# Kernel tuning notes

Hardware: AMD Instinct MI355X
Metric: run time of the kernel (lower is better)

The kernel has to match this reference:

```python
import jax, jax.numpy as jnp
import numpy as np

MAX_SEQ_LEN = 1024
EMBED_DIM = 64


def setup_inputs() -> dict:
    key = jax.random.key(0)
    k1, k2, k3 = jax.random.split(key, 3)
    B, H, L, D = 2, 16, 1024, EMBED_DIM
    q = jax.random.normal(k1, (B, H, L, D), dtype=jnp.float32)
    k = jax.random.normal(k2, (B, H, L, D), dtype=jnp.float32)
    pos_emb = jax.random.normal(k3, (2 * MAX_SEQ_LEN - 1, D), dtype=jnp.float32)
    return {"q": q, "k": k, "pos_emb": pos_emb}


def reference(q, k, pos_emb):
    q_len = q.shape[2]
    k_len = k.shape[2]
    # relative distance index matrix, shifted and clamped into table range
    idx = jnp.arange(q_len)[:, None] - jnp.arange(k_len)[None, :] + (MAX_SEQ_LEN - 1)
    idx = jnp.clip(idx, 0, 2 * MAX_SEQ_LEN - 2)
    rel_emb = pos_emb[idx]  # [q_len, k_len, D]  (the O(Q*K*D) gather)
    # per-query batched contraction over head dim D
    bias = jnp.einsum('bhqd,qkd->bhqk', q, rel_emb)
    return bias / jnp.sqrt(jnp.asarray(EMBED_DIM, dtype=q.dtype))
```

## Files before the change

### kernel.cpp

```cpp
#include <hip/hip_runtime.h>
#include <hip/hip_bf16.h>
#include <stdint.h>


#define LSEQ 1024
#define DDIM 64

typedef __attribute__((ext_vector_type(8))) short bf16x8;
typedef __attribute__((ext_vector_type(16))) float f32x16;

__device__ __forceinline__ unsigned short f2b(float f) {
  union { float f; unsigned u; } c; c.f = f;
  unsigned u = c.u;
  u += 0x7fffu + ((u >> 16) & 1u);
  return (unsigned short)(u >> 16);
}

__global__ __launch_bounds__(256) void cvt_p_kernel(
    const float4* __restrict__ p4, ushort4* __restrict__ pb) {
  int j = blockIdx.x * 256 + threadIdx.x;
  if (j < 32752) {
    float4 v = p4[j];
    ushort4 o;
    o.x = f2b(v.x); o.y = f2b(v.y); o.z = f2b(v.z); o.w = f2b(v.w);
    pb[j] = o;
  }
}

__global__ __launch_bounds__(256) void rpe_kernel(
    const float* __restrict__ Qf, const short* __restrict__ Pb,
    float* __restrict__ out) {
  __shared__ short lds[4][2][2048];
  const int bid  = (int)blockIdx.x;
  const int q    = ((bid & 7) << 7) + (bid >> 3);
  const int tid  = (int)threadIdx.x;
  const int lane = tid & 63;
  const int wave = tid >> 6;
  const int l31  = lane & 31;
  const int hi   = lane >> 5;
  const int nbase = wave << 8;

  const int lane_off = ((lane >> 3) << 7) + ((((lane & 7) ^ (lane >> 3))) << 4);
  const char* Pc = (const char*)Pb;

  auto STAGE = [&](int tt, int buf) {
    const int lo = q + 992 - nbase - (tt << 5);
    const char* src = Pc + ((size_t)lo << 7) + lane_off;
#pragma unroll
    for (int j = 0; j < 4; ++j)
      __builtin_amdgcn_global_load_lds(
          (const __attribute__((address_space(1))) void*)(src + (j << 10)),
          (__attribute__((address_space(3))) void*)&lds[wave][buf][j << 9],
          16, 0, 0);
  };

  STAGE(0, 0);

  bf16x8 a[4];
  {
    const float* qp = Qf + ((size_t)((l31 << 10) + q)) * DDIM + (hi << 3);
#pragma unroll
    for (int s = 0; s < 4; ++s) {
      float4 u = *(const float4*)(qp + 16 * s);
      float4 v = *(const float4*)(qp + 16 * s + 4);
      bf16x8 t;
      t[0] = (short)f2b(u.x * 0.125f); t[1] = (short)f2b(u.y * 0.125f);
      t[2] = (short)f2b(u.z * 0.125f); t[3] = (short)f2b(u.w * 0.125f);
      t[4] = (short)f2b(v.x * 0.125f); t[5] = (short)f2b(v.y * 0.125f);
      t[6] = (short)f2b(v.z * 0.125f); t[7] = (short)f2b(v.w * 0.125f);
      a[s] = t;
    }
  }

  STAGE(1, 1);

  const int rr = 31 - l31;
  const int rx = rr & 7;

  f32x16 accA, accB;
#pragma unroll
  for (int t = 0; t < 8; ++t) {
    if (t == 0 || t == 1)
      asm volatile("s_waitcnt vmcnt(4)" ::: "memory");
    else if (t == 7)
      asm volatile("s_waitcnt vmcnt(32)" ::: "memory");
    else
      asm volatile("s_waitcnt vmcnt(36)" ::: "memory");

    f32x16& acc = (t & 1) ? accB : accA;
#pragma unroll
    for (int r = 0; r < 16; ++r) acc[r] = 0.0f;

    const short* base = &lds[wave][t & 1][rr << 6];
#pragma unroll
    for (int s = 0; s < 4; ++s) {
      bf16x8 bfr = *(const bf16x8*)(base + (((hi + 2 * s) ^ rx) << 3));
      acc = __builtin_amdgcn_mfma_f32_32x32x16_bf16(a[s], bfr, acc, 0, 0, 0);
    }

    if (t < 6) STAGE(t + 2, t & 1);

    if (t & 1) {
      float* ob = out + ((size_t)hi << 22) + (q << 10) + nbase + ((t - 1) << 5) + l31;
#pragma unroll
      for (int r = 0; r < 16; ++r) {
        const int m = (r & 3) + 8 * (r >> 2);
        ob[(size_t)m << 20]        = accA[r];
        ob[((size_t)m << 20) + 32] = accB[r];
      }
    }
  }
}

extern "C" void kernel_launch(void* const* d_in, const int* in_sizes, int n_in,
                              void* d_out, int out_size, void* d_ws, size_t ws_size,
                              hipStream_t stream) {
  const float* qin = (const float*)d_in[0];
  const float* pin = (const float*)d_in[2];

  short* pb = (short*)d_ws;

  cvt_p_kernel<<<128, 256, 0, stream>>>((const float4*)pin, (ushort4*)pb);
  rpe_kernel<<<1024, 256, 0, stream>>>(qin, pb, (float*)d_out);
}
```

Measured before the change: 34.96 us.

## Fuse pos_emb bf16 conversion into main kernel via register-staged LDS writes

Result: slower. 46.86 us (+34.1%).

```diff
diff --git a/kernel.cpp b/kernel.cpp
--- a/kernel.cpp
+++ b/kernel.cpp
@@ -16,19 +16,8 @@
   return (unsigned short)(u >> 16);
 }
 
-__global__ __launch_bounds__(256) void cvt_p_kernel(
-    const float4* __restrict__ p4, ushort4* __restrict__ pb) {
-  int j = blockIdx.x * 256 + threadIdx.x;
-  if (j < 32752) {
-    float4 v = p4[j];
-    ushort4 o;
-    o.x = f2b(v.x); o.y = f2b(v.y); o.z = f2b(v.z); o.w = f2b(v.w);
-    pb[j] = o;
-  }
-}
-
 __global__ __launch_bounds__(256) void rpe_kernel(
-    const float* __restrict__ Qf, const short* __restrict__ Pb,
+    const float* __restrict__ Qf, const float* __restrict__ Pf,
     float* __restrict__ out) {
   __shared__ short lds[4][2][2048];
   const int bid  = (int)blockIdx.x;
@@ -40,21 +29,35 @@
   const int hi   = lane >> 5;
   const int nbase = wave << 8;
 
-  const int lane_off = ((lane >> 3) << 7) + ((((lane & 7) ^ (lane >> 3))) << 4);
-  const char* Pc = (const char*)Pb;
+  const int rl = lane >> 1;
+  const int hl = lane & 1;
+  const int sw = rl & 7;
+  const float4* P4 = (const float4*)Pf;
+  const size_t base4 = ((size_t)(q + 992 - nbase + rl) << 4) + (hl << 3);
 
-  auto STAGE = [&](int tt, int buf) {
-    const int lo = q + 992 - nbase - (tt << 5);
-    const char* src = Pc + ((size_t)lo << 7) + lane_off;
+  float4 pr[8];
+  auto LOADB = [&](int tt) {
+    const float4* s = P4 + (base4 - ((size_t)tt << 9));
 #pragma unroll
-    for (int j = 0; j < 4; ++j)
-      __builtin_amdgcn_global_load_lds(
-          (const __attribute__((address_space(1))) void*)(src + (j << 10)),
-          (__attribute__((address_space(3))) void*)&lds[wave][buf][j << 9],
-          16, 0, 0);
+    for (int j = 0; j < 8; ++j) pr[j] = s[j];
+  };
+  auto WRITEB = [&](int buf) {
+    short* dst = &lds[wave][buf][rl << 6];
+#pragma unroll
+    for (int j = 0; j < 4; ++j) {
+      const float4 u = pr[2 * j], v = pr[2 * j + 1];
+      bf16x8 w;
+      w[0] = (short)f2b(u.x); w[1] = (short)f2b(u.y);
+      w[2] = (short)f2b(u.z); w[3] = (short)f2b(u.w);
+      w[4] = (short)f2b(v.x); w[5] = (short)f2b(v.y);
+      w[6] = (short)f2b(v.z); w[7] = (short)f2b(v.w);
+      *(bf16x8*)(dst + (((((hl << 2) + j)) ^ sw) << 3)) = w;
+    }
   };
 
-  STAGE(0, 0);
+  LOADB(0);
+  WRITEB(0);
+  LOADB(1);
 
   bf16x8 a[4];
   {
@@ -72,20 +75,14 @@
     }
   }
 
-  STAGE(1, 1);
-
   const int rr = 31 - l31;
   const int rx = rr & 7;
 
   f32x16 accA, accB;
 #pragma unroll
   for (int t = 0; t < 8; ++t) {
-    if (t == 0 || t == 1)
-      asm volatile("s_waitcnt vmcnt(4)" ::: "memory");
-    else if (t == 7)
-      asm volatile("s_waitcnt vmcnt(32)" ::: "memory");
-    else
-      asm volatile("s_waitcnt vmcnt(36)" ::: "memory");
+    if (t < 7) WRITEB((t + 1) & 1);
+    if (t < 6) LOADB(t + 2);
 
     f32x16& acc = (t & 1) ? accB : accA;
 #pragma unroll
@@ -97,8 +94,6 @@
       bf16x8 bfr = *(const bf16x8*)(base + (((hi + 2 * s) ^ rx) << 3));
       acc = __builtin_amdgcn_mfma_f32_32x32x16_bf16(a[s], bfr, acc, 0, 0, 0);
     }
-
-    if (t < 6) STAGE(t + 2, t & 1);
 
     if (t & 1) {
       float* ob = out + ((size_t)hi << 22) + (q << 10) + nbase + ((t - 1) << 5) + l31;
@@ -117,9 +112,7 @@
                               hipStream_t stream) {
   const float* qin = (const float*)d_in[0];
   const float* pin = (const float*)d_in[2];
+  (void)d_ws; (void)ws_size;
 
-  short* pb = (short*)d_ws;
-
-  cvt_p_kernel<<<128, 256, 0, stream>>>((const float4*)pin, (ushort4*)pb);
-  rpe_kernel<<<1024, 256, 0, stream>>>(qin, pb, (float*)d_out);
+  rpe_kernel<<<1024, 256, 0, stream>>>(qin, pin, (float*)d_out);
 }
```
